# Optimization experiments

Measured on AMD Instinct MI355X. Metric: run time of the kernel, lower is better.

## Reference

```python
import jax, jax.numpy as jnp
import numpy as np

H = 128  # hidden_size

def _band_agg(h):
    # Equivalent to bmm(adj, h) with adj = degree-normalized tridiagonal
    # (self + left + right neighbor), degree=3 interior, 2 at endpoints,
    # normalization adj/(deg+1e-8) as in the torch module.
    B, S, D = h.shape
    hp = jnp.pad(h, ((0, 0), (1, 1), (0, 0)))
    s = hp[:, :-2] + hp[:, 1:-1] + hp[:, 2:]            # [B,S,D] neighbor sum
    deg = jnp.full((S,), 3.0, dtype=h.dtype).at[0].set(2.0).at[S - 1].set(2.0)
    return s / (deg + 1e-8)[None, :, None]


def setup_inputs() -> dict:
    key = jax.random.key(0)
    ks = jax.random.split(key, 16)
    f32 = jnp.float32
    p = lambda k, shp: (jax.random.normal(k, shp, dtype=f32) * 0.05)
    return {
        "x": jax.random.normal(ks[0], (32, 2048, 6), dtype=f32),
        "enc_w1": p(ks[1], (6, H)),   "enc_b1": p(ks[2], (H,)),
        "enc_w2": p(ks[3], (H, H)),   "enc_b2": p(ks[4], (H,)),
        "gc1_w": p(ks[5], (H, H)),    "gc1_b": p(ks[6], (H,)),
        "gc2_w": p(ks[7], (H, H)),    "gc2_b": p(ks[8], (H,)),
        "gc3_w": p(ks[9], (H, H)),    "gc3_b": p(ks[10], (H,)),
        "cls_w1": p(ks[11], (H, H // 2)), "cls_b1": p(ks[12], (H // 2,)),
        "cls_w2": p(ks[13], (H // 2, 3)), "cls_b2": p(ks[14], (3,)),
    }


def reference(x, enc_w1, enc_b1, enc_w2, enc_b2,
              gc1_w, gc1_b, gc2_w, gc2_b, gc3_w, gc3_b,
              cls_w1, cls_b1, cls_w2, cls_b2):
    # node encoder: Linear -> ReLU -> Linear
    h = jax.nn.relu(x @ enc_w1 + enc_b1) @ enc_w2 + enc_b2
    # three graph convolutions: linear, normalized tridiagonal aggregate, relu
    h = jax.nn.relu(_band_agg(h @ gc1_w + gc1_b))
    h = jax.nn.relu(_band_agg(h @ gc2_w + gc2_b))
    h = jax.nn.relu(_band_agg(h @ gc3_w + gc3_b))
    # AdaptiveAvgPool1d(1) over seq dim after transpose == mean over nodes
    pooled = h.mean(axis=1)                              # [B, H]
    # classifier (dropout inactive in eval)
    return jax.nn.relu(pooled @ cls_w1 + cls_b1) @ cls_w2 + cls_b2
```

## Files before the change

### kernel.cpp

```cpp
#include <hip/hip_runtime.h>

#define SEQ  2048
#define HID  128
#define NB   32
#define TILE 58
#define GX   36
#define MSTR 67

typedef float f2    __attribute__((ext_vector_type(2)));
typedef float f32x4 __attribute__((ext_vector_type(4)));
typedef short bf16x8 __attribute__((ext_vector_type(8)));

__device__ __forceinline__ void split_bf16(float v, short& h, short& l) {
  unsigned u = __float_as_uint(v);
  unsigned r = (u + 0x7fffu + ((u >> 16) & 1u)) >> 16;
  h = (short)r;
  const float hf = __uint_as_float(r << 16);
  const float lo = v - hf;
  unsigned u2 = __float_as_uint(lo);
  unsigned r2 = (u2 + 0x7fffu + ((u2 >> 16) & 1u)) >> 16;
  l = (short)r2;
}

__global__ __launch_bounds__(256) void prep_fold(
    const float* __restrict__ enc_w2, const float* __restrict__ enc_b2,
    const float* __restrict__ gc1_w, const float* __restrict__ gc1_b,
    float* __restrict__ Wp, float* __restrict__ bp)
{
  const int tid = threadIdx.x;
  if (blockIdx.x < 16) {
    const int r = blockIdx.x * 8 + (tid >> 5);
    const int c = (tid & 31) * 4;
    float4 a = make_float4(0.f, 0.f, 0.f, 0.f);
    for (int k = 0; k < 128; ++k) {
      const float w = enc_w2[r * 128 + k];
      const float4 g = *(const float4*)&gc1_w[k * 128 + c];
      a.x = fmaf(w, g.x, a.x); a.y = fmaf(w, g.y, a.y);
      a.z = fmaf(w, g.z, a.z); a.w = fmaf(w, g.w, a.w);
    }
    *(float4*)&Wp[r * 128 + c] = a;
  } else if (tid < 128) {
    float s = gc1_b[tid];
    for (int k = 0; k < 128; ++k) s = fmaf(enc_b2[k], gc1_w[k * 128 + tid], s);
    bp[tid] = s;
  }
}

__global__ __launch_bounds__(256) void prep_shuffle(
    const float* __restrict__ Wp, const float* __restrict__ gc2_w,
    const float* __restrict__ gc3_w, short* __restrict__ Wf)
{
  const int L = blockIdx.y;
  const float* SW = (L == 0) ? Wp : (L == 1) ? gc2_w : gc3_w;
  const int ks = blockIdx.x >> 3, nt = blockIdx.x & 7;
  short* hi = Wf + L * 32768;
  short* lo = hi + 16384;
  for (int f = threadIdx.x; f < 512; f += 256) {
    const int l = f >> 3, j = f & 7;
    const int k = ks * 32 + (l >> 4) * 8 + j;
    const int n = nt * 16 + (l & 15);
    short h, lw;
    split_bf16(SW[k * 128 + n], h, lw);
    const int d = ((ks * 8 + nt) * 64 + l) * 8 + j;
    hi[d] = h; lo[d] = lw;
  }
}

__global__ __launch_bounds__(256) void fused_kernel(
    const float* __restrict__ x,
    const float* __restrict__ enc_w1, const float* __restrict__ enc_b1,
    const short* __restrict__ Wf, const float* __restrict__ bp,
    const float* __restrict__ gc2_b, const float* __restrict__ gc3_b,
    float* __restrict__ partial)
{
  __shared__ float hT[HID * MSTR];
  __shared__ float wsmall[7 * HID];
  __shared__ float psum[256];

  const int tid  = threadIdx.x;
  const int lane = tid & 63;
  const int w    = tid >> 6;
  const int gxb  = blockIdx.x, b = blockIdx.y;
  const int s0   = gxb * TILE;

  for (int f = tid; f < 7 * HID; f += 256)
    wsmall[f] = (f < 6 * HID) ? enc_w1[f] : enc_b1[f - 6 * HID];

  const int sm = s0 - 3 + lane;
  float xv[6];
  if (sm >= 0 && sm < SEQ) {
    const f2* xp = (const f2*)(x + ((long long)b * SEQ + sm) * 6);
    const f2 a0 = xp[0], a1 = xp[1], a2 = xp[2];
    xv[0] = a0.x; xv[1] = a0.y; xv[2] = a1.x;
    xv[3] = a1.y; xv[4] = a2.x; xv[5] = a2.y;
  } else {
    #pragma unroll
    for (int k = 0; k < 6; ++k) xv[k] = 0.f;
  }
  __syncthreads();
  {
    const int c0 = w * 32;
    float4 a4[8];
    #pragma unroll
    for (int q = 0; q < 8; ++q) a4[q] = make_float4(0.f, 0.f, 0.f, 0.f);
    #pragma unroll
    for (int k = 0; k < 6; ++k) {
      #pragma unroll
      for (int q = 0; q < 8; ++q) {
        const float4 wv = *(const float4*)&wsmall[k * HID + c0 + q * 4];
        a4[q].x = fmaf(xv[k], wv.x, a4[q].x);
        a4[q].y = fmaf(xv[k], wv.y, a4[q].y);
        a4[q].z = fmaf(xv[k], wv.z, a4[q].z);
        a4[q].w = fmaf(xv[k], wv.w, a4[q].w);
      }
    }
    #pragma unroll
    for (int q = 0; q < 8; ++q) {
      const float4 bb = *(const float4*)&wsmall[6 * HID + c0 + q * 4];
      const int c = c0 + q * 4;
      hT[(c + 0) * MSTR + lane] = fmaxf(a4[q].x + bb.x, 0.f);
      hT[(c + 1) * MSTR + lane] = fmaxf(a4[q].y + bb.y, 0.f);
      hT[(c + 2) * MSTR + lane] = fmaxf(a4[q].z + bb.z, 0.f);
      hT[(c + 3) * MSTR + lane] = fmaxf(a4[q].w + bb.w, 0.f);
    }
  }
  __syncthreads();

  const int mt   = w * 16 + (lane & 15);
  const int koct = (lane >> 4) * 8;
  const int stt  = s0 - 3 + mt;
  const float invdA = (stt == 0 || stt == SEQ - 1) ? (1.0f / (2.0f + 1e-8f))
                                                   : (1.0f / (3.0f + 1e-8f));
  const int mm = (mt == 0) ? 0 : mt - 1;
  const int mp = (mt == 63) ? 63 : mt + 1;

  #pragma unroll 1
  for (int L = 0; L < 3; ++L) {
    const short* WfL = Wf + L * 32768;
    const bf16x8* Bhi = (const bf16x8*)WfL;
    const bf16x8* Blo = (const bf16x8*)(WfL + 16384);
    const float* bias = (L == 0) ? bp : (L == 1) ? gc2_b : gc3_b;

    f32x4 acc[8];
    #pragma unroll
    for (int nt = 0; nt < 8; ++nt) acc[nt] = (f32x4){0.f, 0.f, 0.f, 0.f};

    #pragma unroll 1
    for (int ks = 0; ks < 4; ++ks) {
      const int fb = ks * 512 + lane;
      bf16x8 bh[8], bl[8];
      #pragma unroll
      for (int nt = 0; nt < 8; ++nt) {
        bh[nt] = Bhi[fb + nt * 64];
        bl[nt] = Blo[fb + nt * 64];
      }
      bf16x8 ah, al;
      const float* pa = &hT[(ks * 32 + koct) * MSTR];
      #pragma unroll
      for (int j = 0; j < 8; ++j) {
        float v;
        if (L == 0) {
          v = pa[j * MSTR + mt];
        } else {
          v = (pa[j * MSTR + mm] + pa[j * MSTR + mt] + pa[j * MSTR + mp]) * invdA;
          v = fmaxf(v, 0.f);
        }
        short h, lo;
        split_bf16(v, h, lo);
        ah[j] = h; al[j] = lo;
      }
      #pragma unroll
      for (int nt = 0; nt < 8; ++nt) {
        acc[nt] = __builtin_amdgcn_mfma_f32_16x16x32_bf16(ah, bh[nt], acc[nt], 0, 0, 0);
        acc[nt] = __builtin_amdgcn_mfma_f32_16x16x32_bf16(ah, bl[nt], acc[nt], 0, 0, 0);
        acc[nt] = __builtin_amdgcn_mfma_f32_16x16x32_bf16(al, bh[nt], acc[nt], 0, 0, 0);
      }
    }
    __syncthreads();

    {
      const int n0 = lane & 15;
      const int mrow0 = w * 16 + (lane >> 4) * 4;
      #pragma unroll
      for (int nt = 0; nt < 8; ++nt) {
        const float bn = bias[nt * 16 + n0];
        float* pw = &hT[(nt * 16 + n0) * MSTR];
        #pragma unroll
        for (int r = 0; r < 4; ++r) {
          const int m = mrow0 + r;
          const int s = s0 - 3 + m;
          const bool vld = (s >= 0 && s < SEQ);
          pw[m] = vld ? (acc[nt][r] + bn) : 0.f;
        }
      }
    }
    __syncthreads();
  }

  {
    const int c = tid & 127, half = tid >> 7;
    float ps = 0.f;
    const float* pc = &hT[c * MSTR];
    #pragma unroll 1
    for (int r = 0; r < 29; ++r) {
      const int m = 3 + half * 29 + r;
      const int s = s0 + half * 29 + r;
      if (s < SEQ) {
        const float invd = (s == 0 || s == SEQ - 1) ? (1.0f / (2.0f + 1e-8f))
                                                    : (1.0f / (3.0f + 1e-8f));
        ps += fmaxf((pc[m - 1] + pc[m] + pc[m + 1]) * invd, 0.f);
      }
    }
    psum[tid] = ps;
  }
  __syncthreads();
  if (tid < 128)
    partial[((long long)b * GX + gxb) * HID + tid] = psum[tid] + psum[tid + 128];
}

__global__ __launch_bounds__(128) void cls_kernel(
    const float* __restrict__ partial,
    const float* __restrict__ w1, const float* __restrict__ b1,
    const float* __restrict__ w2, const float* __restrict__ b2,
    float* __restrict__ out)
{
  __shared__ float ms[128];
  __shared__ float hid[64];
  const int b = blockIdx.x, tid = threadIdx.x;
  float a = 0.f;
  #pragma unroll 1
  for (int g = 0; g < GX; ++g) a += partial[((long long)b * GX + g) * HID + tid];
  ms[tid] = a * (1.0f / 2048.0f);
  __syncthreads();
  if (tid < 64) {
    float h = b1[tid];
    for (int k = 0; k < 128; ++k) h = fmaf(ms[k], w1[k * 64 + tid], h);
    hid[tid] = fmaxf(h, 0.f);
  }
  __syncthreads();
  if (tid < 3) {
    float o = b2[tid];
    for (int k = 0; k < 64; ++k) o = fmaf(hid[k], w2[k * 3 + tid], o);
    out[b * 3 + tid] = o;
  }
}

extern "C" void kernel_launch(void* const* d_in, const int* in_sizes, int n_in,
                              void* d_out, int out_size, void* d_ws, size_t ws_size,
                              hipStream_t stream) {
  (void)in_sizes; (void)n_in; (void)out_size; (void)ws_size;
  const float* x      = (const float*)d_in[0];
  const float* enc_w1 = (const float*)d_in[1];
  const float* enc_b1 = (const float*)d_in[2];
  const float* enc_w2 = (const float*)d_in[3];
  const float* enc_b2 = (const float*)d_in[4];
  const float* gc1_w  = (const float*)d_in[5];
  const float* gc1_b  = (const float*)d_in[6];
  const float* gc2_w  = (const float*)d_in[7];
  const float* gc2_b  = (const float*)d_in[8];
  const float* gc3_w  = (const float*)d_in[9];
  const float* gc3_b  = (const float*)d_in[10];
  const float* cls_w1 = (const float*)d_in[11];
  const float* cls_b1 = (const float*)d_in[12];
  const float* cls_w2 = (const float*)d_in[13];
  const float* cls_b2 = (const float*)d_in[14];

  float* Wp      = (float*)d_ws;
  float* bpv     = Wp + 16384;
  short* Wfrag   = (short*)(bpv + 128);
  float* partial = (float*)(Wfrag + 3 * 2 * 16384);

  prep_fold<<<dim3(17), 256, 0, stream>>>(enc_w2, enc_b2, gc1_w, gc1_b, Wp, bpv);
  prep_shuffle<<<dim3(32, 3), 256, 0, stream>>>(Wp, gc2_w, gc3_w, Wfrag);
  fused_kernel<<<dim3(GX, NB), 256, 0, stream>>>(
      x, enc_w1, enc_b1, Wfrag, bpv, gc2_b, gc3_b, partial);
  cls_kernel<<<dim3(NB), 128, 0, stream>>>(partial, cls_w1, cls_b1, cls_w2, cls_b2,
                                           (float*)d_out);
}
```

Measured before the change: 145.0 us.

## Merge prep kernels and fold classifier into main kernel via last-block atomics

The weight fold (enc_w2·gc1_w) and the bf16 hi/lo fragment shuffle now run in a single prep kernel, with the fold computed per output tile through shared memory. The separate classifier kernel is removed. Each block atomically adds its pooled partial into a per-batch accumulator, and the last block for each batch, found by an atomic counter, runs the classifier. This removes two kernel launches and the partial-buffer round trip. In exchange it adds float atomics, which make the summation order nondeterministic, plus a fence and counter per block.

```diff
diff --git a/kernel.cpp b/kernel.cpp
--- a/kernel.cpp
+++ b/kernel.cpp
@@ -22,47 +22,70 @@
   l = (short)r2;
 }
 
-__global__ __launch_bounds__(256) void prep_fold(
+__global__ __launch_bounds__(256) void prep_kernel(
     const float* __restrict__ enc_w2, const float* __restrict__ enc_b2,
     const float* __restrict__ gc1_w, const float* __restrict__ gc1_b,
-    float* __restrict__ Wp, float* __restrict__ bp)
+    const float* __restrict__ gc2_w, const float* __restrict__ gc3_w,
+    short* __restrict__ Wf, float* __restrict__ bp,
+    float* __restrict__ acc, unsigned* __restrict__ cnt)
 {
   const int tid = threadIdx.x;
-  if (blockIdx.x < 16) {
-    const int r = blockIdx.x * 8 + (tid >> 5);
-    const int c = (tid & 31) * 4;
-    float4 a = make_float4(0.f, 0.f, 0.f, 0.f);
-    for (int k = 0; k < 128; ++k) {
-      const float w = enc_w2[r * 128 + k];
-      const float4 g = *(const float4*)&gc1_w[k * 128 + c];
-      a.x = fmaf(w, g.x, a.x); a.y = fmaf(w, g.y, a.y);
-      a.z = fmaf(w, g.z, a.z); a.w = fmaf(w, g.w, a.w);
-    }
-    *(float4*)&Wp[r * 128 + c] = a;
-  } else if (tid < 128) {
-    float s = gc1_b[tid];
-    for (int k = 0; k < 128; ++k) s = fmaf(enc_b2[k], gc1_w[k * 128 + tid], s);
-    bp[tid] = s;
-  }
-}
-
-__global__ __launch_bounds__(256) void prep_shuffle(
-    const float* __restrict__ Wp, const float* __restrict__ gc2_w,
-    const float* __restrict__ gc3_w, short* __restrict__ Wf)
-{
-  const int L = blockIdx.y;
-  const float* SW = (L == 0) ? Wp : (L == 1) ? gc2_w : gc3_w;
-  const int ks = blockIdx.x >> 3, nt = blockIdx.x & 7;
+  const int bid = blockIdx.x;
+
+  if (bid == 96) {
+    if (tid < 128) {
+      float s = gc1_b[tid];
+      for (int k = 0; k < 128; ++k) s = fmaf(enc_b2[k], gc1_w[k * 128 + tid], s);
+      bp[tid] = s;
+    }
+    for (int i = tid; i < NB * HID; i += 256) acc[i] = 0.f;
+    if (tid < NB) cnt[tid] = 0u;
+    return;
+  }
+
+  const int L = bid >> 5, bx = bid & 31;
   short* hi = Wf + L * 32768;
   short* lo = hi + 16384;
-  for (int f = threadIdx.x; f < 512; f += 256) {
-    const int l = f >> 3, j = f & 7;
-    const int k = ks * 32 + (l >> 4) * 8 + j;
-    const int n = nt * 16 + (l & 15);
-    short h, lw;
-    split_bf16(SW[k * 128 + n], h, lw);
-    const int d = ((ks * 8 + nt) * 64 + l) * 8 + j;
-    hi[d] = h; lo[d] = lw;
+
+  if (L == 0) {
+    __shared__ float As[32 * 128];
+    __shared__ float Bs[128 * 16];
+    const int k0 = (bx >> 3) * 32, n0 = (bx & 7) * 16;
+    for (int i = tid; i < 1024; i += 256)
+      ((f32x4*)As)[i] = ((const f32x4*)(enc_w2 + k0 * 128))[i];
+    for (int i = tid; i < 512; i += 256) {
+      const int t = i >> 2, q = i & 3;
+      ((f32x4*)Bs)[i] = *(const f32x4*)(gc1_w + t * 128 + n0 + q * 4);
+    }
+    __syncthreads();
+    #pragma unroll
+    for (int e = 0; e < 2; ++e) {
+      const int f = tid + e * 256;
+      const int l = f >> 3, j = f & 7;
+      const float* ar = As + ((l >> 4) * 8 + j) * 128;
+      const int nn = l & 15;
+      float s0 = 0.f, s1 = 0.f, s2 = 0.f, s3 = 0.f;
+      for (int t = 0; t < 128; t += 4) {
+        s0 = fmaf(ar[t + 0], Bs[(t + 0) * 16 + nn], s0);
+        s1 = fmaf(ar[t + 1], Bs[(t + 1) * 16 + nn], s1);
+        s2 = fmaf(ar[t + 2], Bs[(t + 2) * 16 + nn], s2);
+        s3 = fmaf(ar[t + 3], Bs[(t + 3) * 16 + nn], s3);
+      }
+      short h, lw;
+      split_bf16((s0 + s1) + (s2 + s3), h, lw);
+      hi[bx * 512 + f] = h; lo[bx * 512 + f] = lw;
+    }
+  } else {
+    const float* __restrict__ SW = (L == 1) ? gc2_w : gc3_w;
+    const int ks = bx >> 3, nt = bx & 7;
+    for (int f = tid; f < 512; f += 256) {
+      const int l = f >> 3, j = f & 7;
+      const int k = ks * 32 + (l >> 4) * 8 + j;
+      const int n = nt * 16 + (l & 15);
+      short h, lw;
+      split_bf16(SW[k * 128 + n], h, lw);
+      hi[bx * 512 + f] = h; lo[bx * 512 + f] = lw;
+    }
   }
 }
 
@@ -71,11 +94,15 @@
     const float* __restrict__ enc_w1, const float* __restrict__ enc_b1,
     const short* __restrict__ Wf, const float* __restrict__ bp,
     const float* __restrict__ gc2_b, const float* __restrict__ gc3_b,
-    float* __restrict__ partial)
+    float* __restrict__ acc, unsigned* __restrict__ cnt,
+    const float* __restrict__ cls_w1, const float* __restrict__ cls_b1,
+    const float* __restrict__ cls_w2, const float* __restrict__ cls_b2,
+    float* __restrict__ out)
 {
   __shared__ float hT[HID * MSTR];
   __shared__ float wsmall[7 * HID];
   __shared__ float psum[256];
+  __shared__ int lastf;
 
   const int tid  = threadIdx.x;
   const int lane = tid & 63;
@@ -141,9 +168,9 @@
     const bf16x8* Blo = (const bf16x8*)(WfL + 16384);
     const float* bias = (L == 0) ? bp : (L == 1) ? gc2_b : gc3_b;
 
-    f32x4 acc[8];
-    #pragma unroll
-    for (int nt = 0; nt < 8; ++nt) acc[nt] = (f32x4){0.f, 0.f, 0.f, 0.f};
+    f32x4 acc_[8];
+    #pragma unroll
+    for (int nt = 0; nt < 8; ++nt) acc_[nt] = (f32x4){0.f, 0.f, 0.f, 0.f};
 
     #pragma unroll 1
     for (int ks = 0; ks < 4; ++ks) {
@@ -171,9 +198,9 @@
       }
       #pragma unroll
       for (int nt = 0; nt < 8; ++nt) {
-        acc[nt] = __builtin_amdgcn_mfma_f32_16x16x32_bf16(ah, bh[nt], acc[nt], 0, 0, 0);
-        acc[nt] = __builtin_amdgcn_mfma_f32_16x16x32_bf16(ah, bl[nt], acc[nt], 0, 0, 0);
-        acc[nt] = __builtin_amdgcn_mfma_f32_16x16x32_bf16(al, bh[nt], acc[nt], 0, 0, 0);
+        acc_[nt] = __builtin_amdgcn_mfma_f32_16x16x32_bf16(ah, bh[nt], acc_[nt], 0, 0, 0);
+        acc_[nt] = __builtin_amdgcn_mfma_f32_16x16x32_bf16(ah, bl[nt], acc_[nt], 0, 0, 0);
+        acc_[nt] = __builtin_amdgcn_mfma_f32_16x16x32_bf16(al, bh[nt], acc_[nt], 0, 0, 0);
       }
     }
     __syncthreads();
@@ -190,7 +217,7 @@
           const int m = mrow0 + r;
           const int s = s0 - 3 + m;
           const bool vld = (s >= 0 && s < SEQ);
-          pw[m] = vld ? (acc[nt][r] + bn) : 0.f;
+          pw[m] = vld ? (acc_[nt][r] + bn) : 0.f;
         }
       }
     }
@@ -214,33 +241,33 @@
     psum[tid] = ps;
   }
   __syncthreads();
+
   if (tid < 128)
-    partial[((long long)b * GX + gxb) * HID + tid] = psum[tid] + psum[tid + 128];
-}
-
-__global__ __launch_bounds__(128) void cls_kernel(
-    const float* __restrict__ partial,
-    const float* __restrict__ w1, const float* __restrict__ b1,
-    const float* __restrict__ w2, const float* __restrict__ b2,
-    float* __restrict__ out)
-{
-  __shared__ float ms[128];
-  __shared__ float hid[64];
-  const int b = blockIdx.x, tid = threadIdx.x;
-  float a = 0.f;
-  #pragma unroll 1
-  for (int g = 0; g < GX; ++g) a += partial[((long long)b * GX + g) * HID + tid];
-  ms[tid] = a * (1.0f / 2048.0f);
+    atomicAdd(&acc[(long long)b * HID + tid], psum[tid] + psum[tid + 128]);
+  __syncthreads();
+  if (tid == 0) {
+    __threadfence();
+    unsigned old = atomicAdd(&cnt[b], 1u);
+    lastf = (old == GX - 1) ? 1 : 0;
+  }
+  __syncthreads();
+  if (!lastf) return;
+
+  if (tid < 128) {
+    const float v = __hip_atomic_load(&acc[(long long)b * HID + tid],
+                                      __ATOMIC_RELAXED, __HIP_MEMORY_SCOPE_AGENT);
+    psum[tid] = v * (1.0f / 2048.0f);
+  }
   __syncthreads();
   if (tid < 64) {
-    float h = b1[tid];
-    for (int k = 0; k < 128; ++k) h = fmaf(ms[k], w1[k * 64 + tid], h);
-    hid[tid] = fmaxf(h, 0.f);
+    float h = cls_b1[tid];
+    for (int k = 0; k < 128; ++k) h = fmaf(psum[k], cls_w1[k * 64 + tid], h);
+    psum[128 + tid] = fmaxf(h, 0.f);
   }
   __syncthreads();
   if (tid < 3) {
-    float o = b2[tid];
-    for (int k = 0; k < 64; ++k) o = fmaf(hid[k], w2[k * 3 + tid], o);
+    float o = cls_b2[tid];
+    for (int k = 0; k < 64; ++k) o = fmaf(psum[128 + k], cls_w2[k * 3 + tid], o);
     out[b * 3 + tid] = o;
   }
 }
@@ -265,15 +292,14 @@
   const float* cls_w2 = (const float*)d_in[13];
   const float* cls_b2 = (const float*)d_in[14];
 
-  float* Wp      = (float*)d_ws;
-  float* bpv     = Wp + 16384;
+  float* bpv     = (float*)d_ws;
   short* Wfrag   = (short*)(bpv + 128);
-  float* partial = (float*)(Wfrag + 3 * 2 * 16384);
-
-  prep_fold<<<dim3(17), 256, 0, stream>>>(enc_w2, enc_b2, gc1_w, gc1_b, Wp, bpv);
-  prep_shuffle<<<dim3(32, 3), 256, 0, stream>>>(Wp, gc2_w, gc3_w, Wfrag);
+  float* accb    = (float*)(Wfrag + 3 * 2 * 16384);
+  unsigned* cntb = (unsigned*)(accb + NB * HID);
+
+  prep_kernel<<<dim3(97), 256, 0, stream>>>(enc_w2, enc_b2, gc1_w, gc1_b,
+                                            gc2_w, gc3_w, Wfrag, bpv, accb, cntb);
   fused_kernel<<<dim3(GX, NB), 256, 0, stream>>>(
-      x, enc_w1, enc_b1, Wfrag, bpv, gc2_b, gc3_b, partial);
-  cls_kernel<<<dim3(NB), 128, 0, stream>>>(partial, cls_w1, cls_b1, cls_w2, cls_b2,
-                                           (float*)d_out);
+      x, enc_w1, enc_b1, Wfrag, bpv, gc2_b, gc3_b, accb, cntb,
+      cls_w1, cls_b1, cls_w2, cls_b2, (float*)d_out);
 }
```

Measured after the change: 147.4 us. About the same (+1.7%).
